# Kernel tuning notes

Measured on AMD Instinct MI355X. Metric: run time of the kernel, lower is better.

Reference implementation:

```python
import jax, jax.numpy as jnp
import numpy as np

N, D, K, H = 100000, 128, 16, 8
EPS = 1e-5


def setup_inputs() -> dict:
    key = jax.random.key(0)
    ks = jax.random.split(key, 8)
    s = 0.02
    return {
        "x": jax.random.normal(ks[0], (N, D), jnp.float32),
        "attention_samples": jax.random.randint(ks[1], (N, K), 0, N),
        "in_proj_w": jax.random.normal(ks[2], (3 * D, D), jnp.float32) * s,
        "in_proj_b": jnp.zeros((3 * D,), jnp.float32),
        "out_w": jax.random.normal(ks[3], (D, D), jnp.float32) * s,
        "out_b": jnp.zeros((D,), jnp.float32),
        "w1": jax.random.normal(ks[4], (4 * D, D), jnp.float32) * s,
        "b1": jnp.zeros((4 * D,), jnp.float32),
        "w2": jax.random.normal(ks[5], (D, 4 * D), jnp.float32) * s,
        "b2": jnp.zeros((D,), jnp.float32),
        "g1": jnp.ones((D,), jnp.float32),
        "be1": jnp.zeros((D,), jnp.float32),
        "g2": jnp.ones((D,), jnp.float32),
        "be2": jnp.zeros((D,), jnp.float32),
    }


def _layernorm(x, g, b):
    m = jnp.mean(x, axis=-1, keepdims=True)
    v = jnp.mean(jnp.square(x - m), axis=-1, keepdims=True)
    return (x - m) * jax.lax.rsqrt(v + EPS) * g + b


def reference(x, attention_samples, in_proj_w, in_proj_b, out_w, out_b,
              w1, b1, w2, b2, g1, be1, g2, be2):
    n, d = x.shape
    h = H
    hd = d // h
    wq, wk, wv = jnp.split(in_proj_w, 3, axis=0)
    bq, bk, bv = jnp.split(in_proj_b, 3, axis=0)
    # per-node query (q_len = 1)
    q = (x @ wq.T + bq).reshape(n, h, hd)            # [N,H,hd]
    samp = x[attention_samples]                       # [N,K,D] gathered neighbors
    k_ = (samp @ wk.T + bk).reshape(n, -1, h, hd)     # [N,K,H,hd]
    v_ = (samp @ wv.T + bv).reshape(n, -1, h, hd)
    scores = jnp.einsum('nhd,nkhd->nhk', q, k_) / jnp.sqrt(jnp.float32(hd))
    attn = jax.nn.softmax(scores, axis=-1)
    ctx = jnp.einsum('nhk,nkhd->nhd', attn, v_).reshape(n, d)
    attn_out = ctx @ out_w.T + out_b
    y = _layernorm(x + attn_out, g1, be1)
    ff = jax.nn.relu(y @ w1.T + b1) @ w2.T + b2
    return _layernorm(y + ff, g2, be2)
```

## Files before the change

### kernel.cpp

```cpp
#include <hip/hip_runtime.h>
#include <hip/hip_bf16.h>

typedef __attribute__((ext_vector_type(8))) short short8;
typedef __attribute__((ext_vector_type(4))) float f32x4;
typedef __attribute__((ext_vector_type(2))) float f32x2;

#define EPS 1e-5f

__device__ __forceinline__ unsigned short f2bf(float f) {
    union { float f; unsigned u; } v; v.f = f;
    unsigned u = v.u;
    u += 0x7FFFu + ((u >> 16) & 1u);
    return (unsigned short)(u >> 16);
}
__device__ __forceinline__ float bflo(unsigned u) {
    union { unsigned u; float f; } v; v.u = u << 16; return v.f;
}
__device__ __forceinline__ float bfhi(unsigned u) {
    union { unsigned u; float f; } v; v.u = u & 0xffff0000u; return v.f;
}
__device__ __forceinline__ float bf2f(ushort u) {
    union { unsigned u; float f; } v; v.u = ((unsigned)u) << 16; return v.f;
}
__device__ __forceinline__ unsigned char f2fp8(float v) {
    return (unsigned char)(__builtin_amdgcn_cvt_pk_fp8_f32(v, v, 0, false) & 0xff);
}
__device__ __forceinline__ int sig(int p) {
    return (((p >> 2) & 1) << 4) | (((p >> 3) & 3) << 2) | (p & 3);
}

__device__ __forceinline__ float dot16_q_k8(const ushort* q, const unsigned char* kp) {
    uint4 kw = *(const uint4*)kp;
    const unsigned* qd = (const unsigned*)q;
    f32x2 a, b; float s = 0.f;
    a = __builtin_amdgcn_cvt_pk_f32_fp8(kw.x, false);
    b = __builtin_amdgcn_cvt_pk_f32_fp8(kw.x, true);
    s += a[0]*bflo(qd[0]) + a[1]*bfhi(qd[0]) + b[0]*bflo(qd[1]) + b[1]*bfhi(qd[1]);
    a = __builtin_amdgcn_cvt_pk_f32_fp8(kw.y, false);
    b = __builtin_amdgcn_cvt_pk_f32_fp8(kw.y, true);
    s += a[0]*bflo(qd[2]) + a[1]*bfhi(qd[2]) + b[0]*bflo(qd[3]) + b[1]*bfhi(qd[3]);
    a = __builtin_amdgcn_cvt_pk_f32_fp8(kw.z, false);
    b = __builtin_amdgcn_cvt_pk_f32_fp8(kw.z, true);
    s += a[0]*bflo(qd[4]) + a[1]*bfhi(qd[4]) + b[0]*bflo(qd[5]) + b[1]*bfhi(qd[5]);
    a = __builtin_amdgcn_cvt_pk_f32_fp8(kw.w, false);
    b = __builtin_amdgcn_cvt_pk_f32_fp8(kw.w, true);
    s += a[0]*bflo(qd[6]) + a[1]*bfhi(qd[6]) + b[0]*bflo(qd[7]) + b[1]*bfhi(qd[7]);
    return s;
}

__global__ __launch_bounds__(256) void k_prep(
        const float* __restrict__ ipw, const float* __restrict__ ow,
        const float* __restrict__ w1, const float* __restrict__ w2,
        const float* __restrict__ x,
        ushort* __restrict__ wqb, ushort* __restrict__ wobs,
        ushort* __restrict__ w1s, ushort* __restrict__ w2t,
        ushort* __restrict__ xb, int nx) {
    int i = blockIdx.x * 256 + threadIdx.x;
    if (i < 49152) wqb[i] = f2bf(ipw[i]);
    if (i < 16384) {
        int r = i >> 7, k16 = (i >> 3) & 15, e = i & 7;
        wobs[i] = f2bf(ow[r*128 + ((k16 ^ (r & 7)) << 3) + e]);
    }
    if (i < 65536) {
        {
            int kb = i >> 12, r = (i >> 7) & 31, k16 = (i >> 3) & 15, e = i & 7;
            int cp = ((k16 ^ (r & 7)) << 3) + e;
            int cs = (cp & ~31) | sig(cp & 31);
            w1s[i] = f2bf(w1[(kb*32 + r)*128 + cs]);
        }
        {
            int kb = i >> 12, chunk = (i >> 10) & 3, row = (i >> 3) & 127, e = i & 7;
            w2t[i] = f2bf(w2[row*512 + kb*32 + sig(chunk*8 + e)]);
        }
    }
    int stride = gridDim.x * 256 * 4;
    for (int j = i * 4; j < nx; j += stride) {
        f32x4 v = *(const f32x4*)(x + j);
        uint2 o;
        o.x = (unsigned)f2bf(v[0]) | ((unsigned)f2bf(v[1]) << 16);
        o.y = (unsigned)f2bf(v[2]) | ((unsigned)f2bf(v[3]) << 16);
        *(uint2*)(xb + j) = o;
    }
}

__global__ __launch_bounds__(256) void k_qkv(
        const ushort* __restrict__ xb, const ushort* __restrict__ w,
        const float* __restrict__ bias, ushort* __restrict__ qt,
        unsigned char* __restrict__ kv8, int N) {
    const int wave = threadIdx.x >> 6, lane = threadIdx.x & 63;
    const int l16 = lane & 15, l4 = lane >> 4;
    const int base = blockIdx.x * 64;

    short8 af[4][4];
    #pragma unroll
    for (int mt = 0; mt < 4; ++mt) {
        int row = base + mt*16 + l16;
        int rc = row < N ? row : N - 1;
        const ushort* p = xb + (size_t)rc*128 + l4*8;
        #pragma unroll
        for (int kb = 0; kb < 4; ++kb) af[mt][kb] = *(const short8*)(p + kb*32);
    }
    #pragma unroll
    for (int i = 0; i < 6; ++i) {
        int col = (wave*6 + i)*16 + l16;
        const ushort* pw = w + (size_t)col*128 + l4*8;
        short8 bf[4];
        #pragma unroll
        for (int kb = 0; kb < 4; ++kb) bf[kb] = *(const short8*)(pw + kb*32);
        float bv = bias[col];
        #pragma unroll
        for (int mt = 0; mt < 4; ++mt) {
            f32x4 acc = {0.f, 0.f, 0.f, 0.f};
            #pragma unroll
            for (int kb = 0; kb < 4; ++kb)
                acc = __builtin_amdgcn_mfma_f32_16x16x32_bf16(af[mt][kb], bf[kb], acc, 0, 0, 0);
            #pragma unroll
            for (int r = 0; r < 4; ++r) {
                int row = base + mt*16 + l4*4 + r;
                if (row < N) {
                    float v = acc[r] + bv;
                    if (col < 128) qt[(size_t)row*128 + col] = f2bf(v);
                    else kv8[(size_t)row*256 + (col - 128)] = f2fp8(v);
                }
            }
        }
    }
}

__global__ __launch_bounds__(256) void k_attn(
        ushort* __restrict__ qt, const unsigned char* __restrict__ kv8,
        const int* __restrict__ samp, int N) {
    __shared__ float aw[4][8][17];
    __shared__ int   ai[4][16];
    const int wave = threadIdx.x >> 6, lane = threadIdx.x & 63;
    const int n = blockIdx.x * 4 + wave;
    if (n >= N) return;
    const int k  = lane & 15;
    const int hp = lane >> 4;
    const int h0 = hp, h1 = hp + 4;

    const int idx = samp[(size_t)n*16 + k];
    const ushort* qrow = qt + (size_t)n*128;
    const unsigned char* krow = kv8 + (size_t)idx*256;

    float s0 = dot16_q_k8(qrow + h0*16, krow + h0*16);
    float s1 = dot16_q_k8(qrow + h1*16, krow + h1*16);
    s0 *= 0.25f; s1 *= 0.25f;
    float m0 = s0, m1 = s1;
    #pragma unroll
    for (int off = 1; off < 16; off <<= 1) {
        m0 = fmaxf(m0, __shfl_xor(m0, off));
        m1 = fmaxf(m1, __shfl_xor(m1, off));
    }
    float e0 = __expf(s0 - m0), e1 = __expf(s1 - m1);
    float d0 = e0, d1 = e1;
    #pragma unroll
    for (int off = 1; off < 16; off <<= 1) {
        d0 += __shfl_xor(d0, off);
        d1 += __shfl_xor(d1, off);
    }
    aw[wave][h0][k] = e0 / d0;
    aw[wave][h1][k] = e1 / d1;
    if (hp == 0) ai[wave][k] = idx;

    const int c = lane & 15;
    const int g = lane >> 4;
    const int h = c >> 1;

    int rows[4];
    #pragma unroll
    for (int b = 0; b < 4; ++b) rows[b] = ai[wave][g + b*4];
    uint2 vv[4];
    #pragma unroll
    for (int b = 0; b < 4; ++b)
        vv[b] = *(const uint2*)(kv8 + (size_t)(unsigned)rows[b]*256 + 128 + c*8);
    float wk[4];
    #pragma unroll
    for (int b = 0; b < 4; ++b) wk[b] = aw[wave][h][g + b*4];

    float a8[8] = {0.f,0.f,0.f,0.f,0.f,0.f,0.f,0.f};
    #pragma unroll
    for (int b = 0; b < 4; ++b) {
        f32x2 p;
        p = __builtin_amdgcn_cvt_pk_f32_fp8(vv[b].x, false);
        a8[0] = fmaf(wk[b], p[0], a8[0]); a8[1] = fmaf(wk[b], p[1], a8[1]);
        p = __builtin_amdgcn_cvt_pk_f32_fp8(vv[b].x, true);
        a8[2] = fmaf(wk[b], p[0], a8[2]); a8[3] = fmaf(wk[b], p[1], a8[3]);
        p = __builtin_amdgcn_cvt_pk_f32_fp8(vv[b].y, false);
        a8[4] = fmaf(wk[b], p[0], a8[4]); a8[5] = fmaf(wk[b], p[1], a8[5]);
        p = __builtin_amdgcn_cvt_pk_f32_fp8(vv[b].y, true);
        a8[6] = fmaf(wk[b], p[0], a8[6]); a8[7] = fmaf(wk[b], p[1], a8[7]);
    }
    #pragma unroll
    for (int i = 0; i < 8; ++i) {
        a8[i] += __shfl_xor(a8[i], 16);
        a8[i] += __shfl_xor(a8[i], 32);
    }
    if (lane < 16) {
        uint4 pack;
        pack.x = (unsigned)f2bf(a8[0]) | ((unsigned)f2bf(a8[1]) << 16);
        pack.y = (unsigned)f2bf(a8[2]) | ((unsigned)f2bf(a8[3]) << 16);
        pack.z = (unsigned)f2bf(a8[4]) | ((unsigned)f2bf(a8[5]) << 16);
        pack.w = (unsigned)f2bf(a8[6]) | ((unsigned)f2bf(a8[7]) << 16);
        *(uint4*)(qt + (size_t)n*128 + c*8) = pack;
    }
}

__global__ __launch_bounds__(256) void k_tail(
        const ushort* __restrict__ ctx, const float* __restrict__ ob,
        const ushort* __restrict__ xb,
        const float* __restrict__ g1, const float* __restrict__ be1,
        const ushort* __restrict__ wobs, const ushort* __restrict__ w1s,
        const float* __restrict__ b1, const ushort* __restrict__ w2t,
        const float* __restrict__ b2,
        const float* __restrict__ g2, const float* __restrict__ be2,
        float* __restrict__ out, int N) {
    __shared__ __align__(16) char smem[49152];
    const int tid = threadIdx.x;
    const int wave = tid >> 6, lane = tid & 63;
    const int l16 = lane & 15, l4 = lane >> 4;
    const int base = blockIdx.x * 128 + wave * 32;
    int row[2], rc[2];
    row[0] = base + l16;       rc[0] = row[0] < N ? row[0] : N - 1;
    row[1] = base + 16 + l16;  rc[1] = row[1] < N ? row[1] : N - 1;

    {
        uint4 st[8], c0[4];
        const uint4* wo4 = (const uint4*)wobs;
        #pragma unroll
        for (int j = 0; j < 8; ++j) st[j] = wo4[j*256 + tid];
        const uint4* w14 = (const uint4*)w1s;
        const uint4* w24 = (const uint4*)w2t;
        c0[0] = w14[tid]; c0[1] = w14[256 + tid];
        c0[2] = w24[tid]; c0[3] = w24[256 + tid];
        #pragma unroll
        for (int j = 0; j < 8; ++j) *(uint4*)(smem + (j*256 + tid)*16) = st[j];
        *(uint4*)(smem + 32768 + tid*16)               = c0[0];
        *(uint4*)(smem + 32768 + (256 + tid)*16)       = c0[1];
        *(uint4*)(smem + 32768 + 8192 + tid*16)        = c0[2];
        *(uint4*)(smem + 32768 + 8192 + (256 + tid)*16) = c0[3];
    }
    __syncthreads();

    short8 cf[2][4];
    #pragma unroll
    for (int mt = 0; mt < 2; ++mt)
        #pragma unroll
        for (int c = 0; c < 4; ++c)
            cf[mt][c] = *(const short8*)(ctx + (size_t)rc[mt]*128 + c*32 + l4*8);

    f32x4 yv[2][8];
    float sum0 = 0.f, sq0 = 0.f, sum1 = 0.f, sq1 = 0.f;
    #pragma unroll
    for (int nt = 0; nt < 8; ++nt) {
        f32x4 a0 = {0.f,0.f,0.f,0.f}, a1 = {0.f,0.f,0.f,0.f};
        #pragma unroll
        for (int c = 0; c < 4; ++c) {
            int rowi = nt*16 + l16;
            int slot = (c*4 + l4) ^ (l16 & 7);
            short8 wf = *(const short8*)(smem + rowi*256 + slot*16);
            a0 = __builtin_amdgcn_mfma_f32_16x16x32_bf16(wf, cf[0][c], a0, 0, 0, 0);
            a1 = __builtin_amdgcn_mfma_f32_16x16x32_bf16(wf, cf[1][c], a1, 0, 0, 0);
        }
        f32x4 obv = *(const f32x4*)(ob + nt*16 + l4*4);
        uint2 xr0 = *(const uint2*)(xb + (size_t)rc[0]*128 + nt*16 + l4*4);
        uint2 xr1 = *(const uint2*)(xb + (size_t)rc[1]*128 + nt*16 + l4*4);
        yv[0][nt][0] = a0[0] + obv[0] + bflo(xr0.x);
        yv[0][nt][1] = a0[1] + obv[1] + bfhi(xr0.x);
        yv[0][nt][2] = a0[2] + obv[2] + bflo(xr0.y);
        yv[0][nt][3] = a0[3] + obv[3] + bfhi(xr0.y);
        yv[1][nt][0] = a1[0] + obv[0] + bflo(xr1.x);
        yv[1][nt][1] = a1[1] + obv[1] + bfhi(xr1.x);
        yv[1][nt][2] = a1[2] + obv[2] + bflo(xr1.y);
        yv[1][nt][3] = a1[3] + obv[3] + bfhi(xr1.y);
        #pragma unroll
        for (int r = 0; r < 4; ++r) {
            sum0 += yv[0][nt][r]; sq0 += yv[0][nt][r]*yv[0][nt][r];
            sum1 += yv[1][nt][r]; sq1 += yv[1][nt][r]*yv[1][nt][r];
        }
    }
    sum0 += __shfl_xor(sum0, 16); sum0 += __shfl_xor(sum0, 32);
    sq0  += __shfl_xor(sq0, 16);  sq0  += __shfl_xor(sq0, 32);
    sum1 += __shfl_xor(sum1, 16); sum1 += __shfl_xor(sum1, 32);
    sq1  += __shfl_xor(sq1, 16);  sq1  += __shfl_xor(sq1, 32);
    float mean[2], rstd[2];
    mean[0] = sum0 * (1.f/128.f);
    rstd[0] = rsqrtf(sq0*(1.f/128.f) - mean[0]*mean[0] + EPS);
    mean[1] = sum1 * (1.f/128.f);
    rstd[1] = rsqrtf(sq1*(1.f/128.f) - mean[1]*mean[1] + EPS);

    short8 yfrag[2][4];
    #pragma unroll
    for (int nt = 0; nt < 8; ++nt) {
        f32x4 gv = *(const f32x4*)(g1 + nt*16 + l4*4);
        f32x4 bv = *(const f32x4*)(be1 + nt*16 + l4*4);
        #pragma unroll
        for (int mt = 0; mt < 2; ++mt)
            #pragma unroll
            for (int r = 0; r < 4; ++r) {
                float yn = (yv[mt][nt][r] - mean[mt]) * rstd[mt] * gv[r] + bv[r];
                yfrag[mt][nt >> 1][(nt & 1)*4 + r] = (short)f2bf(yn);
            }
    }
    __syncthreads();

    f32x4 acc2[2][8];
    #pragma unroll
    for (int mt = 0; mt < 2; ++mt)
        #pragma unroll
        for (int nt = 0; nt < 8; ++nt) acc2[mt][nt] = (f32x4){0.f,0.f,0.f,0.f};

    #pragma unroll 2
    for (int kb = 0; kb < 16; ++kb) {
        char* cur = smem + ((kb & 1) ? 0 : 32768);
        char* nxt = smem + ((kb & 1) ? 32768 : 0);
        uint4 nx0, nx1, nx2, nx3;
        if (kb < 15) {
            const uint4* w14 = (const uint4*)(w1s + (kb + 1)*4096);
            const uint4* w24 = (const uint4*)(w2t + (kb + 1)*4096);
            nx0 = w14[tid]; nx1 = w14[256 + tid];
            nx2 = w24[tid]; nx3 = w24[256 + tid];
        }
        short8 wA[4], wB[4];
        #pragma unroll
        for (int c = 0; c < 4; ++c) {
            int slot = (c*4 + l4) ^ (l16 & 7);
            wA[c] = *(const short8*)(cur + l16*256 + slot*16);
            wB[c] = *(const short8*)(cur + 4096 + l16*256 + slot*16);
        }
        f32x4 hA[2] = {{0.f,0.f,0.f,0.f},{0.f,0.f,0.f,0.f}};
        f32x4 hB[2] = {{0.f,0.f,0.f,0.f},{0.f,0.f,0.f,0.f}};
        #pragma unroll
        for (int c = 0; c < 4; ++c)
            #pragma unroll
            for (int mt = 0; mt < 2; ++mt) {
                hA[mt] = __builtin_amdgcn_mfma_f32_16x16x32_bf16(wA[c], yfrag[mt][c], hA[mt], 0, 0, 0);
                hB[mt] = __builtin_amdgcn_mfma_f32_16x16x32_bf16(wB[c], yfrag[mt][c], hB[mt], 0, 0, 0);
            }
        f32x4 bA = *(const f32x4*)(b1 + kb*32 + l4*4);
        f32x4 bB = *(const f32x4*)(b1 + kb*32 + 16 + l4*4);
        short8 hf[2];
        #pragma unroll
        for (int mt = 0; mt < 2; ++mt)
            #pragma unroll
            for (int r = 0; r < 4; ++r) {
                float vA = hA[mt][r] + bA[r]; vA = vA > 0.f ? vA : 0.f;
                float vB = hB[mt][r] + bB[r]; vB = vB > 0.f ? vB : 0.f;
                hf[mt][r]     = (short)f2bf(vA);
                hf[mt][4 + r] = (short)f2bf(vB);
            }
        #pragma unroll
        for (int nt = 0; nt < 8; ++nt) {
            short8 w2f = *(const short8*)(cur + 8192 + l4*2048 + (nt*16 + l16)*16);
            acc2[0][nt] = __builtin_amdgcn_mfma_f32_16x16x32_bf16(w2f, hf[0], acc2[0][nt], 0, 0, 0);
            acc2[1][nt] = __builtin_amdgcn_mfma_f32_16x16x32_bf16(w2f, hf[1], acc2[1][nt], 0, 0, 0);
        }
        if (kb < 15) {
            *(uint4*)(nxt + tid*16)               = nx0;
            *(uint4*)(nxt + (256 + tid)*16)       = nx1;
            *(uint4*)(nxt + 8192 + tid*16)        = nx2;
            *(uint4*)(nxt + 8192 + (256 + tid)*16) = nx3;
        }
        __syncthreads();
    }

    #pragma unroll
    for (int mt = 0; mt < 2; ++mt) {
        float sum2 = 0.f, sq2 = 0.f;
        #pragma unroll
        for (int nt = 0; nt < 8; ++nt) {
            f32x4 b2v = *(const f32x4*)(b2 + nt*16 + l4*4);
            #pragma unroll
            for (int r = 0; r < 4; ++r) {
                float s = bf2f((ushort)yfrag[mt][nt >> 1][(nt & 1)*4 + r]) + acc2[mt][nt][r] + b2v[r];
                acc2[mt][nt][r] = s; sum2 += s; sq2 += s*s;
            }
        }
        sum2 += __shfl_xor(sum2, 16); sum2 += __shfl_xor(sum2, 32);
        sq2  += __shfl_xor(sq2, 16);  sq2  += __shfl_xor(sq2, 32);
        float mean2 = sum2 * (1.f/128.f);
        float rstd2 = rsqrtf(sq2*(1.f/128.f) - mean2*mean2 + EPS);
        if (row[mt] < N) {
            #pragma unroll
            for (int nt = 0; nt < 8; ++nt) {
                f32x4 gv = *(const f32x4*)(g2 + nt*16 + l4*4);
                f32x4 bv = *(const f32x4*)(be2 + nt*16 + l4*4);
                f32x4 o;
                #pragma unroll
                for (int r = 0; r < 4; ++r)
                    o[r] = (acc2[mt][nt][r] - mean2) * rstd2 * gv[r] + bv[r];
                *(f32x4*)(out + (size_t)row[mt]*128 + nt*16 + l4*4) = o;
            }
        }
    }
}

extern "C" void kernel_launch(void* const* d_in, const int* in_sizes, int n_in,
                              void* d_out, int out_size, void* d_ws, size_t ws_size,
                              hipStream_t stream) {
    (void)n_in; (void)out_size; (void)ws_size;
    const float* x   = (const float*)d_in[0];
    const int*   smp = (const int*)  d_in[1];
    const float* ipw = (const float*)d_in[2];
    const float* ipb = (const float*)d_in[3];
    const float* ow  = (const float*)d_in[4];
    const float* ob  = (const float*)d_in[5];
    const float* w1  = (const float*)d_in[6];
    const float* b1  = (const float*)d_in[7];
    const float* w2  = (const float*)d_in[8];
    const float* b2  = (const float*)d_in[9];
    const float* g1  = (const float*)d_in[10];
    const float* be1 = (const float*)d_in[11];
    const float* g2  = (const float*)d_in[12];
    const float* be2 = (const float*)d_in[13];
    const int N = in_sizes[0] / 128;

    ushort* qt   = (ushort*)d_ws;
    unsigned char* kv8 = (unsigned char*)(qt + (size_t)N*128);
    ushort* wqb  = (ushort*)(kv8 + (size_t)N*256);
    ushort* wobs = wqb + 384*128;
    ushort* w1s  = wobs + 128*128;
    ushort* w2t  = w1s + 512*128;
    ushort* xb   = w2t + 128*512;
    float*  outp = (float*)d_out;

    const int nb = (N + 63) / 64;
    k_prep <<<12500,       256, 0, stream>>>(ipw, ow, w1, w2, x, wqb, wobs, w1s, w2t, xb, N*128);
    k_qkv  <<<nb,          256, 0, stream>>>(xb, wqb, ipb, qt, kv8, N);
    k_attn <<<(N+3)/4,     256, 0, stream>>>(qt, kv8, smp, N);
    k_tail <<<(N+127)/128, 256, 0, stream>>>(qt, ob, xb, g1, be1,
                                             wobs, w1s, b1, w2t, b2, g2, be2, outp, N);
}
```

Measured before the change: 220.6 us.

## Fuse x bf16 conversion into QKV kernel and stream tail weights through unified pipeline

The separate x-to-bf16 pass in the prep kernel is removed. The QKV kernel now reads fp32 x directly, converts it in registers, and writes the bf16 copy that the tail kernel uses. Tail weights are repacked into one contiguous staged array, so the out-projection weights stream through the same 16KB double buffer as the FFN weights. This cuts shared memory from 48KB to 32KB and adds a launch_bounds hint for 4 blocks per CU, aiming at higher occupancy and a smaller prep launch. The cost is that QKV must load fp32 x, twice the bytes, and k_tail has more pipeline stages and barriers.

```diff
diff --git a/kernel.cpp b/kernel.cpp
--- a/kernel.cpp
+++ b/kernel.cpp
@@ -27,6 +27,17 @@
 }
 __device__ __forceinline__ int sig(int p) {
     return (((p >> 2) & 1) << 4) | (((p >> 3) & 3) << 2) | (p & 3);
+}
+
+__device__ __forceinline__ short8 load_frag_f32(const float* __restrict__ p) {
+    f32x4 a = *(const f32x4*)p;
+    f32x4 b = *(const f32x4*)(p + 4);
+    short8 r;
+    r[0] = (short)f2bf(a[0]); r[1] = (short)f2bf(a[1]);
+    r[2] = (short)f2bf(a[2]); r[3] = (short)f2bf(a[3]);
+    r[4] = (short)f2bf(b[0]); r[5] = (short)f2bf(b[1]);
+    r[6] = (short)f2bf(b[2]); r[7] = (short)f2bf(b[3]);
+    return r;
 }
 
 __device__ __forceinline__ float dot16_q_k8(const ushort* q, const unsigned char* kp) {
@@ -51,42 +62,40 @@
 __global__ __launch_bounds__(256) void k_prep(
         const float* __restrict__ ipw, const float* __restrict__ ow,
         const float* __restrict__ w1, const float* __restrict__ w2,
-        const float* __restrict__ x,
-        ushort* __restrict__ wqb, ushort* __restrict__ wobs,
-        ushort* __restrict__ w1s, ushort* __restrict__ w2t,
-        ushort* __restrict__ xb, int nx) {
+        ushort* __restrict__ wqb, ushort* __restrict__ wcat) {
     int i = blockIdx.x * 256 + threadIdx.x;
     if (i < 49152) wqb[i] = f2bf(ipw[i]);
-    if (i < 16384) {
-        int r = i >> 7, k16 = (i >> 3) & 15, e = i & 7;
-        wobs[i] = f2bf(ow[r*128 + ((k16 ^ (r & 7)) << 3) + e]);
-    }
-    if (i < 65536) {
-        {
-            int kb = i >> 12, r = (i >> 7) & 31, k16 = (i >> 3) & 15, e = i & 7;
-            int cp = ((k16 ^ (r & 7)) << 3) + e;
-            int cs = (cp & ~31) | sig(cp & 31);
-            w1s[i] = f2bf(w1[(kb*32 + r)*128 + cs]);
-        }
-        {
-            int kb = i >> 12, chunk = (i >> 10) & 3, row = (i >> 3) & 127, e = i & 7;
-            w2t[i] = f2bf(w2[row*512 + kb*32 + sig(chunk*8 + e)]);
-        }
-    }
-    int stride = gridDim.x * 256 * 4;
-    for (int j = i * 4; j < nx; j += stride) {
-        f32x4 v = *(const f32x4*)(x + j);
-        uint2 o;
-        o.x = (unsigned)f2bf(v[0]) | ((unsigned)f2bf(v[1]) << 16);
-        o.y = (unsigned)f2bf(v[2]) | ((unsigned)f2bf(v[3]) << 16);
-        *(uint2*)(xb + j) = o;
+    if (i < 147456) {
+        float v;
+        if (i < 8192) {
+            int r = i >> 6, s = (i >> 3) & 7, e = i & 7;
+            v = ow[r*128 + ((s ^ (r & 7)) << 3) + e];
+        } else if (i < 16384) {
+            int j = i - 8192;
+            int r = j >> 6, s = (j >> 3) & 7, e = j & 7;
+            v = ow[r*128 + 64 + ((s ^ (r & 7)) << 3) + e];
+        } else {
+            int j = i - 16384;
+            int kb = j >> 13, o = j & 8191;
+            if (o < 4096) {
+                int r = (o >> 7) & 31, k16 = (o >> 3) & 15, e = o & 7;
+                int cp = ((k16 ^ (r & 7)) << 3) + e;
+                int cs = (cp & ~31) | sig(cp & 31);
+                v = w1[(kb*32 + r)*128 + cs];
+            } else {
+                int oo = o - 4096;
+                int ch = (oo >> 10) & 3, rw = (oo >> 3) & 127, e = oo & 7;
+                v = w2[rw*512 + kb*32 + sig(ch*8 + e)];
+            }
+        }
+        wcat[i] = f2bf(v);
     }
 }
 
 __global__ __launch_bounds__(256) void k_qkv(
-        const ushort* __restrict__ xb, const ushort* __restrict__ w,
+        const float* __restrict__ x, const ushort* __restrict__ w,
         const float* __restrict__ bias, ushort* __restrict__ qt,
-        unsigned char* __restrict__ kv8, int N) {
+        unsigned char* __restrict__ kv8, ushort* __restrict__ xb, int N) {
     const int wave = threadIdx.x >> 6, lane = threadIdx.x & 63;
     const int l16 = lane & 15, l4 = lane >> 4;
     const int base = blockIdx.x * 64;
@@ -96,9 +105,18 @@
     for (int mt = 0; mt < 4; ++mt) {
         int row = base + mt*16 + l16;
         int rc = row < N ? row : N - 1;
-        const ushort* p = xb + (size_t)rc*128 + l4*8;
-        #pragma unroll
-        for (int kb = 0; kb < 4; ++kb) af[mt][kb] = *(const short8*)(p + kb*32);
+        const float* p = x + (size_t)rc*128 + l4*8;
+        #pragma unroll
+        for (int kb = 0; kb < 4; ++kb) af[mt][kb] = load_frag_f32(p + kb*32);
+    }
+    #pragma unroll
+    for (int mt = 0; mt < 4; ++mt) {
+        int row = base + mt*16 + l16;
+        if (row < N) {
+            #pragma unroll
+            for (int kb = 0; kb < 4; ++kb)
+                *(short8*)(xb + (size_t)row*128 + kb*32 + l4*8) = af[mt][kb];
+        }
     }
     #pragma unroll
     for (int i = 0; i < 6; ++i) {
@@ -206,77 +224,81 @@
     }
 }
 
-__global__ __launch_bounds__(256) void k_tail(
+__global__ __launch_bounds__(256, 4) void k_tail(
         const ushort* __restrict__ ctx, const float* __restrict__ ob,
         const ushort* __restrict__ xb,
         const float* __restrict__ g1, const float* __restrict__ be1,
-        const ushort* __restrict__ wobs, const ushort* __restrict__ w1s,
-        const float* __restrict__ b1, const ushort* __restrict__ w2t,
+        const ushort* __restrict__ wcat, const float* __restrict__ b1,
         const float* __restrict__ b2,
         const float* __restrict__ g2, const float* __restrict__ be2,
         float* __restrict__ out, int N) {
-    __shared__ __align__(16) char smem[49152];
+    __shared__ __align__(16) char smem[32768];
     const int tid = threadIdx.x;
-    const int wave = tid >> 6, lane = tid & 63;
+    const int lane = tid & 63;
     const int l16 = lane & 15, l4 = lane >> 4;
-    const int base = blockIdx.x * 128 + wave * 32;
+    const int base = blockIdx.x * 128 + (tid >> 6) * 32;
     int row[2], rc[2];
     row[0] = base + l16;       rc[0] = row[0] < N ? row[0] : N - 1;
     row[1] = base + 16 + l16;  rc[1] = row[1] < N ? row[1] : N - 1;
 
-    {
-        uint4 st[8], c0[4];
-        const uint4* wo4 = (const uint4*)wobs;
-        #pragma unroll
-        for (int j = 0; j < 8; ++j) st[j] = wo4[j*256 + tid];
-        const uint4* w14 = (const uint4*)w1s;
-        const uint4* w24 = (const uint4*)w2t;
-        c0[0] = w14[tid]; c0[1] = w14[256 + tid];
-        c0[2] = w24[tid]; c0[3] = w24[256 + tid];
-        #pragma unroll
-        for (int j = 0; j < 8; ++j) *(uint4*)(smem + (j*256 + tid)*16) = st[j];
-        *(uint4*)(smem + 32768 + tid*16)               = c0[0];
-        *(uint4*)(smem + 32768 + (256 + tid)*16)       = c0[1];
-        *(uint4*)(smem + 32768 + 8192 + tid*16)        = c0[2];
-        *(uint4*)(smem + 32768 + 8192 + (256 + tid)*16) = c0[3];
-    }
+    uint4 nx0, nx1, nx2, nx3;
+    const uint4* wc4 = (const uint4*)wcat;
+#define STAGE_LOAD(cidx) { const uint4* s4 = wc4 + (cidx)*1024; \
+    nx0 = s4[tid]; nx1 = s4[256 + tid]; nx2 = s4[512 + tid]; nx3 = s4[768 + tid]; }
+#define STAGE_WRITE(cidx) { char* d = smem + (((cidx)&1) << 14); \
+    *(uint4*)(d + tid*16) = nx0; *(uint4*)(d + (256 + tid)*16) = nx1; \
+    *(uint4*)(d + (512 + tid)*16) = nx2; *(uint4*)(d + (768 + tid)*16) = nx3; }
+
+    STAGE_LOAD(0); STAGE_WRITE(0); STAGE_LOAD(1);
     __syncthreads();
 
-    short8 cf[2][4];
+    f32x4 acc[2][8];
     #pragma unroll
     for (int mt = 0; mt < 2; ++mt)
         #pragma unroll
-        for (int c = 0; c < 4; ++c)
-            cf[mt][c] = *(const short8*)(ctx + (size_t)rc[mt]*128 + c*32 + l4*8);
-
-    f32x4 yv[2][8];
+        for (int nt = 0; nt < 8; ++nt) acc[mt][nt] = (f32x4){0.f,0.f,0.f,0.f};
+
+    #pragma unroll
+    for (int ph = 0; ph < 2; ++ph) {
+        STAGE_WRITE(ph + 1); STAGE_LOAD(ph + 2);
+        short8 cfp[2][2];
+        #pragma unroll
+        for (int mt = 0; mt < 2; ++mt)
+            #pragma unroll
+            for (int j = 0; j < 2; ++j)
+                cfp[mt][j] = *(const short8*)(ctx + (size_t)rc[mt]*128 + (ph*2 + j)*32 + l4*8);
+        char* cur = smem + ((ph & 1) << 14);
+        #pragma unroll
+        for (int nt = 0; nt < 8; ++nt) {
+            #pragma unroll
+            for (int j = 0; j < 2; ++j) {
+                int slot = (j*4 + l4) ^ (l16 & 7);
+                short8 wf = *(const short8*)(cur + (nt*16 + l16)*128 + slot*16);
+                acc[0][nt] = __builtin_amdgcn_mfma_f32_16x16x32_bf16(wf, cfp[0][j], acc[0][nt], 0, 0, 0);
+                acc[1][nt] = __builtin_amdgcn_mfma_f32_16x16x32_bf16(wf, cfp[1][j], acc[1][nt], 0, 0, 0);
+            }
+        }
+        __syncthreads();
+    }
+
     float sum0 = 0.f, sq0 = 0.f, sum1 = 0.f, sq1 = 0.f;
     #pragma unroll
     for (int nt = 0; nt < 8; ++nt) {
-        f32x4 a0 = {0.f,0.f,0.f,0.f}, a1 = {0.f,0.f,0.f,0.f};
-        #pragma unroll
-        for (int c = 0; c < 4; ++c) {
-            int rowi = nt*16 + l16;
-            int slot = (c*4 + l4) ^ (l16 & 7);
-            short8 wf = *(const short8*)(smem + rowi*256 + slot*16);
-            a0 = __builtin_amdgcn_mfma_f32_16x16x32_bf16(wf, cf[0][c], a0, 0, 0, 0);
-            a1 = __builtin_amdgcn_mfma_f32_16x16x32_bf16(wf, cf[1][c], a1, 0, 0, 0);
-        }
         f32x4 obv = *(const f32x4*)(ob + nt*16 + l4*4);
         uint2 xr0 = *(const uint2*)(xb + (size_t)rc[0]*128 + nt*16 + l4*4);
         uint2 xr1 = *(const uint2*)(xb + (size_t)rc[1]*128 + nt*16 + l4*4);
-        yv[0][nt][0] = a0[0] + obv[0] + bflo(xr0.x);
-        yv[0][nt][1] = a0[1] + obv[1] + bfhi(xr0.x);
-        yv[0][nt][2] = a0[2] + obv[2] + bflo(xr0.y);
-        yv[0][nt][3] = a0[3] + obv[3] + bfhi(xr0.y);
-        yv[1][nt][0] = a1[0] + obv[0] + bflo(xr1.x);
-        yv[1][nt][1] = a1[1] + obv[1] + bfhi(xr1.x);
-        yv[1][nt][2] = a1[2] + obv[2] + bflo(xr1.y);
-        yv[1][nt][3] = a1[3] + obv[3] + bfhi(xr1.y);
+        acc[0][nt][0] += obv[0] + bflo(xr0.x);
+        acc[0][nt][1] += obv[1] + bfhi(xr0.x);
+        acc[0][nt][2] += obv[2] + bflo(xr0.y);
+        acc[0][nt][3] += obv[3] + bfhi(xr0.y);
+        acc[1][nt][0] += obv[0] + bflo(xr1.x);
+        acc[1][nt][1] += obv[1] + bfhi(xr1.x);
+        acc[1][nt][2] += obv[2] + bflo(xr1.y);
+        acc[1][nt][3] += obv[3] + bfhi(xr1.y);
         #pragma unroll
         for (int r = 0; r < 4; ++r) {
-            sum0 += yv[0][nt][r]; sq0 += yv[0][nt][r]*yv[0][nt][r];
-            sum1 += yv[1][nt][r]; sq1 += yv[1][nt][r]*yv[1][nt][r];
+            sum0 += acc[0][nt][r]; sq0 += acc[0][nt][r]*acc[0][nt][r];
+            sum1 += acc[1][nt][r]; sq1 += acc[1][nt][r]*acc[1][nt][r];
         }
     }
     sum0 += __shfl_xor(sum0, 16); sum0 += __shfl_xor(sum0, 32);
@@ -298,29 +320,23 @@
         for (int mt = 0; mt < 2; ++mt)
             #pragma unroll
             for (int r = 0; r < 4; ++r) {
-                float yn = (yv[mt][nt][r] - mean[mt]) * rstd[mt] * gv[r] + bv[r];
+                float yn = (acc[mt][nt][r] - mean[mt]) * rstd[mt] * gv[r] + bv[r];
                 yfrag[mt][nt >> 1][(nt & 1)*4 + r] = (short)f2bf(yn);
             }
     }
-    __syncthreads();
-
-    f32x4 acc2[2][8];
+
+    f32x4 (&acc2)[2][8] = acc;
     #pragma unroll
     for (int mt = 0; mt < 2; ++mt)
         #pragma unroll
         for (int nt = 0; nt < 8; ++nt) acc2[mt][nt] = (f32x4){0.f,0.f,0.f,0.f};
 
     #pragma unroll 2
-    for (int kb = 0; kb < 16; ++kb) {
-        char* cur = smem + ((kb & 1) ? 0 : 32768);
-        char* nxt = smem + ((kb & 1) ? 32768 : 0);
-        uint4 nx0, nx1, nx2, nx3;
-        if (kb < 15) {
-            const uint4* w14 = (const uint4*)(w1s + (kb + 1)*4096);
-            const uint4* w24 = (const uint4*)(w2t + (kb + 1)*4096);
-            nx0 = w14[tid]; nx1 = w14[256 + tid];
-            nx2 = w24[tid]; nx3 = w24[256 + tid];
-        }
+    for (int p = 2; p < 18; ++p) {
+        if (p <= 16) { STAGE_WRITE(p + 1); }
+        if (p <= 15) { STAGE_LOAD(p + 2); }
+        const int kb = p - 2;
+        char* cur = smem + ((p & 1) << 14);
         short8 wA[4], wB[4];
         #pragma unroll
         for (int c = 0; c < 4; ++c) {
@@ -355,13 +371,7 @@
             acc2[0][nt] = __builtin_amdgcn_mfma_f32_16x16x32_bf16(w2f, hf[0], acc2[0][nt], 0, 0, 0);
             acc2[1][nt] = __builtin_amdgcn_mfma_f32_16x16x32_bf16(w2f, hf[1], acc2[1][nt], 0, 0, 0);
         }
-        if (kb < 15) {
-            *(uint4*)(nxt + tid*16)               = nx0;
-            *(uint4*)(nxt + (256 + tid)*16)       = nx1;
-            *(uint4*)(nxt + 8192 + tid*16)        = nx2;
-            *(uint4*)(nxt + 8192 + (256 + tid)*16) = nx3;
-        }
-        __syncthreads();
+        if (p < 17) __syncthreads();
     }
 
     #pragma unroll
@@ -393,6 +403,8 @@
             }
         }
     }
+#undef STAGE_LOAD
+#undef STAGE_WRITE
 }
 
 extern "C" void kernel_launch(void* const* d_in, const int* in_sizes, int n_in,
@@ -418,16 +430,13 @@
     ushort* qt   = (ushort*)d_ws;
     unsigned char* kv8 = (unsigned char*)(qt + (size_t)N*128);
     ushort* wqb  = (ushort*)(kv8 + (size_t)N*256);
-    ushort* wobs = wqb + 384*128;
-    ushort* w1s  = wobs + 128*128;
-    ushort* w2t  = w1s + 512*128;
-    ushort* xb   = w2t + 128*512;
+    ushort* wcat = wqb + 384*128;
+    ushort* xb   = wcat + 18*8192;
     float*  outp = (float*)d_out;
 
-    const int nb = (N + 63) / 64;
-    k_prep <<<12500,       256, 0, stream>>>(ipw, ow, w1, w2, x, wqb, wobs, w1s, w2t, xb, N*128);
-    k_qkv  <<<nb,          256, 0, stream>>>(xb, wqb, ipb, qt, kv8, N);
+    k_prep <<<576,         256, 0, stream>>>(ipw, ow, w1, w2, wqb, wcat);
+    k_qkv  <<<(N+63)/64,   256, 0, stream>>>(x, wqb, ipb, qt, kv8, xb, N);
     k_attn <<<(N+3)/4,     256, 0, stream>>>(qt, kv8, smp, N);
     k_tail <<<(N+127)/128, 256, 0, stream>>>(qt, ob, xb, g1, be1,
-                                             wobs, w1s, b1, w2t, b2, g2, be2, outp, N);
-}
+                                             wcat, b1, b2, g2, be2, outp, N);
+}
```

Measured after the change: 335.2 us. +51.9%, slower.
